# Optimization experiments

Hardware: AMD Instinct MI355X
Metric: run time of the kernel (lower is better)

The kernel has to match this reference:

```python
import jax, jax.numpy as jnp
import numpy as np

B, S, CIN, COUT, W, M, P = 32, 8192, 2, 1, 64, 16, 24


def setup_inputs() -> dict:
    key = jax.random.key(0)
    ks = jax.random.split(key, 12)

    def lin(k, o, i):
        return (jax.random.uniform(k, (o, i), jnp.float32) * 2 - 1) / np.float32(np.sqrt(i))

    scale = np.float32(1.0 / (W * W))  # SpectralConv1d init scale 1/(in*out)
    return {
        "x": jax.random.normal(ks[0], (B, S, CIN), jnp.float32),
        "fc0_w": lin(ks[1], W, CIN),
        "fc0_b": jnp.zeros((W,), jnp.float32),
        "conv_wr": jax.random.uniform(ks[2], (4, W, W, M), jnp.float32) * scale,
        "conv_wi": jax.random.uniform(ks[3], (4, W, W, M), jnp.float32) * scale,
        "pw_w": lin(ks[4], 4 * W, W).reshape(4, W, W),  # 1x1 conv weights (out,in)
        "pw_b": jnp.zeros((4, W), jnp.float32),
        "fc1_w": lin(ks[5], 128, W),
        "fc1_b": jnp.zeros((128,), jnp.float32),
        "fc2_w": lin(ks[6], COUT, 128),
        "ica_w": lin(ks[7], P, 128),
        "ica_b": jnp.zeros((P,), jnp.float32),
    }


def spectral_conv(h, wr, wi, n):
    # h: (B, W, S). Keep first M rfft modes, complex-multiply, inverse rfft.
    xf = jnp.fft.rfft(h, axis=-1)[..., :M]          # (B, W, M) complex
    w = wr + 1j * wi                                 # (W, W, M)
    of = jnp.einsum('bix,iox->box', xf, w)           # (B, W, M)
    of = jnp.pad(of, ((0, 0), (0, 0), (0, n // 2 + 1 - M)))
    return jnp.fft.irfft(of, n=n, axis=-1)


def reference(x, fc0_w, fc0_b, conv_wr, conv_wi, pw_w, pw_b, fc1_w, fc1_b, fc2_w, ica_w, ica_b):
    b, s, _ = x.shape
    h = x @ fc0_w.T + fc0_b                          # lift: (B, S, W)
    h = h.transpose(0, 2, 1)                         # (B, W, S)
    for l in range(4):
        x1 = spectral_conv(h, conv_wr[l], conv_wi[l], s)
        x2 = jnp.einsum('oi,bis->bos', pw_w[l], h) + pw_b[l][None, :, None]
        h = x1 + x2
        if l < 3:                                    # no relu after layer 3 (as in torch code)
            h = jax.nn.relu(h)
    h = h.transpose(0, 2, 1)                         # (B, S, W)
    h = h @ fc1_w.T + fc1_b                          # (B, S, 128)
    h_ = jax.nn.relu(h)
    # broadcast ICA decomposition: (B,S,1,128)*(1,1,COUT,128)
    components = h_[:, :, None, :] * fc2_w[None, None, :, :]
    tc = components @ ica_w.T + ica_b                # (B, S, COUT, P)
    out = tc.sum(-1)                                 # (B, S, COUT)
    return out, tc
```

## Files before the change

kernel.cpp:

```cpp
#include <hip/hip_runtime.h>
#include <math.h>

#define SB 8192
#define NB 32
#define WC 64
#define NM 16
#define NKC 32
#define NP 24
#define NSC 16
#define LP 132


__global__ __launch_bounds__(256) void k_table(float* __restrict__ T) {
    int s = blockIdx.x * 256 + threadIdx.x;
    float* row = T + (size_t)s * NKC;
    #pragma unroll
    for (int k = 0; k < NM; ++k) {
        int m = (k * s) & (SB - 1);
        double ang = (double)m * (6.283185307179586476925286766559 / (double)SB);
        row[2 * k]     = (float)cos(ang);
        row[2 * k + 1] = (float)sin(ang);
    }
}

__global__ __launch_bounds__(256) void k_prep(const float* __restrict__ ica_w,
                                              const float* __restrict__ fc2_w,
                                              float* __restrict__ icaT) {
    int tid = blockIdx.x * 256 + threadIdx.x;
    int c = tid / NP;
    int p = tid - c * NP;
    icaT[c * NP + p] = ica_w[p * 128 + c] * fc2_w[c];
}

__global__ __launch_bounds__(256) void k_prepw(const float* __restrict__ pw_w,
                                               float* __restrict__ pwT) {
    int tid = blockIdx.x * 256 + threadIdx.x;
    int l = tid >> 12, k = (tid >> 6) & 63, o = tid & 63;
    pwT[tid] = pw_w[(size_t)l * 4096 + o * 64 + k];
}

__global__ __launch_bounds__(256) void k_lift(const float* __restrict__ x,
                                              const float* __restrict__ fc0_w,
                                              const float* __restrict__ fc0_b,
                                              float* __restrict__ h) {
    int b = blockIdx.y;
    int s = blockIdx.x * 256 + threadIdx.x;
    float2 xv = ((const float2*)x)[(size_t)b * SB + s];
    #pragma unroll
    for (int w = 0; w < WC; ++w) {
        float v = fmaf(xv.x, fc0_w[2 * w], fmaf(xv.y, fc0_w[2 * w + 1], fc0_b[w]));
        h[((size_t)(b * WC + w)) * SB + s] = v;
    }
}

__global__ __launch_bounds__(256) void k_dft(const float* __restrict__ h,
                                             const float* __restrict__ T,
                                             float* __restrict__ xfp) {
    __shared__ float u[12800];
    int blk = blockIdx.x;
    int b  = blk >> 4;
    int sc = blk & (NSC - 1);
    int t  = threadIdx.x;
    int lane = t & 63;
    int wv = __builtin_amdgcn_readfirstlane(t >> 6);
    int g  = lane >> 3;
    int j8 = lane & 7;

    float acc[8][4];
    #pragma unroll
    for (int i = 0; i < 8; ++i)
        #pragma unroll
        for (int m = 0; m < 4; ++m) acc[i][m] = 0.f;

    int ch_s = t >> 2, part = t & 3;
    const float* hb = h + ((size_t)(b * WC + ch_s)) * SB;

    for (int st = 0; st < 4; ++st) {
        int s_base = sc * 512 + st * 128;

        const float* hrow = hb + s_base;
        #pragma unroll
        for (int r = 0; r < 8; ++r) {
            int so = (part + 4 * r) * 4;
            float4 v = *(const float4*)(hrow + so);
            u[(so + 0) * 68 + ch_s] = v.x;
            u[(so + 1) * 68 + ch_s] = v.y;
            u[(so + 2) * 68 + ch_s] = v.z;
            u[(so + 3) * 68 + ch_s] = v.w;
        }
        {
            const float4* tsrc = (const float4*)(T + (size_t)s_base * NKC);
            float4* tdst = (float4*)(u + 8704);
            #pragma unroll
            for (int r = 0; r < 4; ++r) tdst[t + r * 256] = tsrc[t + r * 256];
        }
        __syncthreads();

        #pragma unroll 4
        for (int ss = 0; ss < 32; ++ss) {
            int s = wv * 32 + ss;
            float4 tv = *(const float4*)&u[8704 + s * 32 + j8 * 4];
            float4 h0 = *(const float4*)&u[s * 68 + g * 8];
            float4 h1 = *(const float4*)&u[s * 68 + g * 8 + 4];
            float hh[8] = {h0.x, h0.y, h0.z, h0.w, h1.x, h1.y, h1.z, h1.w};
            #pragma unroll
            for (int i = 0; i < 8; ++i) {
                acc[i][0] = fmaf(hh[i], tv.x, acc[i][0]);
                acc[i][1] = fmaf(hh[i], tv.y, acc[i][1]);
                acc[i][2] = fmaf(hh[i], tv.z, acc[i][2]);
                acc[i][3] = fmaf(hh[i], tv.w, acc[i][3]);
            }
        }
        __syncthreads();
    }

    {
        float* slot = u + (wv * 64 + lane) * 33;
        #pragma unroll
        for (int i = 0; i < 8; ++i)
            #pragma unroll
            for (int m = 0; m < 4; ++m) slot[i * 4 + m] = acc[i][m];
    }
    __syncthreads();

    float* dst = xfp + ((size_t)(sc * NB + b)) * 2048;
    float res[8];
    #pragma unroll
    for (int e = 0; e < 8; ++e) {
        int idx = t * 8 + e;
        int ch = idx >> 5, mode = idx & 31;
        int g2 = ch >> 3, i2 = ch & 7;
        int q2 = mode >> 2, m2 = mode & 3;
        int lane2 = g2 * 8 + q2;
        int v2 = i2 * 4 + m2;
        res[e] = u[lane2 * 33 + v2] + u[(64 + lane2) * 33 + v2]
               + u[(128 + lane2) * 33 + v2] + u[(192 + lane2) * 33 + v2];
    }
    float4* d4 = (float4*)(dst + t * 8);
    d4[0] = make_float4(res[0], res[1], res[2], res[3]);
    d4[1] = make_float4(res[4], res[5], res[6], res[7]);
}

__global__ __launch_bounds__(256) void k_red(const float* __restrict__ xfp,
                                             float* __restrict__ xf) {
    int idx = blockIdx.x * 256 + threadIdx.x;
    int b = idx >> 11;
    int r = idx & 2047;
    float s = 0.f;
    #pragma unroll
    for (int sc = 0; sc < NSC; ++sc)
        s += xfp[((size_t)(sc * NB + b)) * 2048 + r];
    xf[idx] = s;
}

__global__ __launch_bounds__(256) void k_mix(const float* __restrict__ xf,
                                             const float* __restrict__ wr,
                                             const float* __restrict__ wi,
                                             float* __restrict__ ofT) {
    int tid = blockIdx.x * 256 + threadIdx.x;
    int k = tid & 15;
    int o = (tid >> 4) & 63;
    int b = tid >> 10;
    float orr = 0.f, oii = 0.f;
    const float2* xfb = (const float2*)(xf + (size_t)b * WC * NKC);
    #pragma unroll 4
    for (int i = 0; i < WC; ++i) {
        float2 cs = xfb[i * NM + k];
        float wrv = wr[(i * WC + o) * NM + k];
        float wiv = wi[(i * WC + o) * NM + k];
        orr = fmaf(cs.x, wrv, fmaf(cs.y, wiv, orr));
        oii = fmaf(cs.x, wiv, fmaf(-cs.y, wrv, oii));
    }
    float alpha = (k == 0 ? 1.f : 2.f) / (float)SB;
    ofT[((size_t)b * NKC + 2 * k) * 64 + o]     = alpha * orr;
    ofT[((size_t)b * NKC + 2 * k + 1) * 64 + o] = -alpha * oii;
}

__global__ __launch_bounds__(256) void k_update(float* __restrict__ h,
                                                const float* __restrict__ T,
                                                const float* __restrict__ ofT,
                                                const float* __restrict__ pwT,
                                                const float* __restrict__ pwb,
                                                int relu) {
    __shared__ float hS[96][LP];
    int t = threadIdx.x;
    int b = blockIdx.y;
    int s0 = blockIdx.x * 128;
    int lane_s = t & 63;
    int g = __builtin_amdgcn_readfirstlane((t >> 6) & 3);
    int ob = g * 16;

    {
        int ch = t >> 2, part = t & 3;
        const float* hrow = h + ((size_t)(b * WC + ch)) * SB + s0;
        #pragma unroll
        for (int r = 0; r < 8; ++r) {
            int so = (part + 4 * r) * 4;
            *(float4*)&hS[ch][so] = *(const float4*)(hrow + so);
        }
    }
    {
        int sl = t >> 1, jj0 = (t & 1) * 16;
        const float4* src = (const float4*)(T + (size_t)(s0 + sl) * NKC + jj0);
        float4 a = src[0], c4 = src[1], d = src[2], e = src[3];
        hS[64 + jj0 +  0][sl] = a.x;  hS[64 + jj0 +  1][sl] = a.y;
        hS[64 + jj0 +  2][sl] = a.z;  hS[64 + jj0 +  3][sl] = a.w;
        hS[64 + jj0 +  4][sl] = c4.x; hS[64 + jj0 +  5][sl] = c4.y;
        hS[64 + jj0 +  6][sl] = c4.z; hS[64 + jj0 +  7][sl] = c4.w;
        hS[64 + jj0 +  8][sl] = d.x;  hS[64 + jj0 +  9][sl] = d.y;
        hS[64 + jj0 + 10][sl] = d.z;  hS[64 + jj0 + 11][sl] = d.w;
        hS[64 + jj0 + 12][sl] = e.x;  hS[64 + jj0 + 13][sl] = e.y;
        hS[64 + jj0 + 14][sl] = e.z;  hS[64 + jj0 + 15][sl] = e.w;
    }
    __syncthreads();

    float acc0[16], acc1[16];
    #pragma unroll
    for (int o = 0; o < 16; ++o) { acc0[o] = pwb[ob + o]; acc1[o] = pwb[ob + o]; }

    const float* wbase0 = pwT + ob;
    const float* wbase1 = ofT + ((size_t)b * NKC) * 64 + ob;

    for (int kc = 0; kc < 8; ++kc) {
        #pragma unroll
        for (int u = 0; u < 8; ++u) {
            int k = kc * 8 + u;
            float h0 = hS[k][lane_s];
            float h1 = hS[k][64 + lane_s];
            const float* w = wbase0 + k * 64;
            #pragma unroll
            for (int o = 0; o < 16; ++o) {
                acc0[o] = fmaf(w[o], h0, acc0[o]);
                acc1[o] = fmaf(w[o], h1, acc1[o]);
            }
        }
    }
    for (int kc = 0; kc < 4; ++kc) {
        #pragma unroll
        for (int u = 0; u < 8; ++u) {
            int j = kc * 8 + u;
            float h0 = hS[64 + j][lane_s];
            float h1 = hS[64 + j][64 + lane_s];
            const float* w = wbase1 + j * 64;
            #pragma unroll
            for (int o = 0; o < 16; ++o) {
                acc0[o] = fmaf(w[o], h0, acc0[o]);
                acc1[o] = fmaf(w[o], h1, acc1[o]);
            }
        }
    }

    float* hw0 = h + (size_t)b * WC * SB + s0 + lane_s;
    float* hw1 = hw0 + 64;
    #pragma unroll
    for (int o = 0; o < 16; ++o) {
        float v0 = acc0[o], v1 = acc1[o];
        if (relu) { v0 = fmaxf(v0, 0.f); v1 = fmaxf(v1, 0.f); }
        hw0[(size_t)(ob + o) * SB] = v0;
        hw1[(size_t)(ob + o) * SB] = v1;
    }
}

__global__ __launch_bounds__(256) void k_final(const float* __restrict__ h,
                                               const float* __restrict__ fc1_w,
                                               const float* __restrict__ fc1_b,
                                               const float* __restrict__ icaT,
                                               const float* __restrict__ ica_b,
                                               float* __restrict__ out,
                                               float* __restrict__ tc) {
    __shared__ float u_lds[6400];
    float (*hS)[68] = (float(*)[68])u_lds;
    int t = threadIdx.x;
    int b = blockIdx.y;
    int s0 = blockIdx.x * 64;
    int lane_s = t & 63;
    int wv = __builtin_amdgcn_readfirstlane(t >> 6);
    int c0 = wv * 32;

    {
        int sl = t & 63, chg = t >> 6;
        const float* hb = h + (size_t)b * WC * SB + s0 + sl;
        #pragma unroll
        for (int cc = 0; cc < 16; ++cc) {
            int ch = chg * 16 + cc;
            hS[sl][ch] = hb[(size_t)ch * SB];
        }
    }
    __syncthreads();

    float acc[NP];
    #pragma unroll
    for (int p = 0; p < NP; ++p) acc[p] = 0.f;

    for (int cq = 0; cq < 8; ++cq) {
        int c = c0 + 4 * cq;
        float tv0 = fc1_b[c], tv1 = fc1_b[c + 1], tv2 = fc1_b[c + 2], tv3 = fc1_b[c + 3];
        const float* w0 = fc1_w + (size_t)c * WC;
        const float* w1 = w0 + WC;
        const float* w2 = w1 + WC;
        const float* w3 = w2 + WC;
        for (int ioct = 0; ioct < 8; ++ioct) {
            float4 xa = *(const float4*)&hS[lane_s][ioct * 8];
            float4 xb = *(const float4*)&hS[lane_s][ioct * 8 + 4];
            float xs[8] = {xa.x, xa.y, xa.z, xa.w, xb.x, xb.y, xb.z, xb.w};
            #pragma unroll
            for (int u = 0; u < 8; ++u) {
                int i = ioct * 8 + u;
                tv0 = fmaf(w0[i], xs[u], tv0);
                tv1 = fmaf(w1[i], xs[u], tv1);
                tv2 = fmaf(w2[i], xs[u], tv2);
                tv3 = fmaf(w3[i], xs[u], tv3);
            }
        }
        tv0 = fmaxf(tv0, 0.f); tv1 = fmaxf(tv1, 0.f);
        tv2 = fmaxf(tv2, 0.f); tv3 = fmaxf(tv3, 0.f);
        const float* e0 = icaT + (size_t)c * NP;
        const float* e1 = e0 + NP;
        const float* e2 = e1 + NP;
        const float* e3 = e2 + NP;
        #pragma unroll
        for (int p = 0; p < NP; ++p)
            acc[p] = fmaf(tv0, e0[p], fmaf(tv1, e1[p],
                     fmaf(tv2, e2[p], fmaf(tv3, e3[p], acc[p]))));
    }

    __syncthreads();
    {
        float* slot = u_lds + ((t >> 6) * 64 + lane_s) * 25;
        #pragma unroll
        for (int p = 0; p < NP; ++p) slot[p] = acc[p];
    }
    __syncthreads();

    float* tcb = tc + ((size_t)b * SB + s0) * NP;
    #pragma unroll
    for (int r = 0; r < 6; ++r) {
        int e = t + r * 256;
        int s = e / NP, p = e - s * NP;
        float v = u_lds[s * 25 + p] + u_lds[(64 + s) * 25 + p]
                + u_lds[(128 + s) * 25 + p] + u_lds[(192 + s) * 25 + p]
                + ica_b[p];
        tcb[e] = v;
        u_lds[s * 25 + p] = v;
    }
    __syncthreads();
    if (t < 64) {
        float osum = 0.f;
        #pragma unroll
        for (int p = 0; p < NP; ++p) osum += u_lds[t * 25 + p];
        out[(size_t)b * SB + s0 + t] = osum;
    }
}

extern "C" void kernel_launch(void* const* d_in, const int* in_sizes, int n_in,
                              void* d_out, int out_size, void* d_ws, size_t ws_size,
                              hipStream_t stream) {
    const float* x     = (const float*)d_in[0];
    const float* fc0_w = (const float*)d_in[1];
    const float* fc0_b = (const float*)d_in[2];
    const float* cwr   = (const float*)d_in[3];
    const float* cwi   = (const float*)d_in[4];
    const float* pw_w  = (const float*)d_in[5];
    const float* pw_b  = (const float*)d_in[6];
    const float* fc1_w = (const float*)d_in[7];
    const float* fc1_b = (const float*)d_in[8];
    const float* fc2_w = (const float*)d_in[9];
    const float* ica_w = (const float*)d_in[10];
    const float* ica_b = (const float*)d_in[11];

    float* out = (float*)d_out;
    float* tc  = out + (size_t)NB * SB;

    float* ws   = (float*)d_ws;
    float* h    = ws;
    float* T    = ws + 16777216;
    float* xf   = ws + 17039360;
    float* ofT  = ws + 17104896;
    float* icaT = ws + 17170432;
    float* pwT  = ws + 17173504;
    float* xfp  = tc;

    k_table<<<32, 256, 0, stream>>>(T);
    k_prep<<<12, 256, 0, stream>>>(ica_w, fc2_w, icaT);
    k_prepw<<<64, 256, 0, stream>>>(pw_w, pwT);
    k_lift<<<dim3(32, 32), 256, 0, stream>>>(x, fc0_w, fc0_b, h);

    for (int l = 0; l < 4; ++l) {
        k_dft<<<NB * NSC, 256, 0, stream>>>(h, T, xfp);
        k_red<<<256, 256, 0, stream>>>(xfp, xf);
        k_mix<<<128, 256, 0, stream>>>(xf, cwr + (size_t)l * WC * WC * NM,
                                       cwi + (size_t)l * WC * WC * NM, ofT);
        k_update<<<dim3(64, 32), 256, 0, stream>>>(h, T, ofT,
                                                   pwT + (size_t)l * 4096,
                                                   pw_b + (size_t)l * WC,
                                                   (l < 3) ? 1 : 0);
    }

    k_final<<<dim3(128, 32), 256, 0, stream>>>(h, fc1_w, fc1_b, icaT, ica_b, out, tc);
}
```

Measured before the change: 434.8 us.

## Fuse forward DFT partial sums into k_update epilogue for next layer

For layers 0-2, k_update now stages its freshly computed h tile in LDS after writing it out. It then computes the 16-mode DFT partial sums for its 128-sample chunk and writes them to xfp. This removes the separate k_dft launch for layers 1-3 and its re-read of the full h tensor from global memory. k_red now takes a variable chunk count (64 instead of 16) to reduce the finer-grained partials. The cost is more LDS work and syncs per block and a larger partial-sum buffer to read.

```diff
diff --git a/kernel.cpp b/kernel.cpp
--- a/kernel.cpp
+++ b/kernel.cpp
@@ -142,13 +142,13 @@
 }
 
 __global__ __launch_bounds__(256) void k_red(const float* __restrict__ xfp,
-                                             float* __restrict__ xf) {
+                                             float* __restrict__ xf, int nsc) {
     int idx = blockIdx.x * 256 + threadIdx.x;
     int b = idx >> 11;
     int r = idx & 2047;
     float s = 0.f;
-    #pragma unroll
-    for (int sc = 0; sc < NSC; ++sc)
+    #pragma unroll 8
+    for (int sc = 0; sc < nsc; ++sc)
         s += xfp[((size_t)(sc * NB + b)) * 2048 + r];
     xf[idx] = s;
 }
@@ -181,14 +181,16 @@
                                                 const float* __restrict__ ofT,
                                                 const float* __restrict__ pwT,
                                                 const float* __restrict__ pwb,
-                                                int relu) {
-    __shared__ float hS[96][LP];
+                                                int relu, float* __restrict__ xfp,
+                                                int dodft) {
+    __shared__ float u[96 * LP];
+    float (*hS)[LP] = (float(*)[LP])u;
     int t = threadIdx.x;
     int b = blockIdx.y;
     int s0 = blockIdx.x * 128;
     int lane_s = t & 63;
-    int g = __builtin_amdgcn_readfirstlane((t >> 6) & 3);
-    int ob = g * 16;
+    int g4 = __builtin_amdgcn_readfirstlane((t >> 6) & 3);
+    int ob = g4 * 16;
 
     {
         int ch = t >> 2, part = t & 3;
@@ -223,8 +225,8 @@
 
     for (int kc = 0; kc < 8; ++kc) {
         #pragma unroll
-        for (int u = 0; u < 8; ++u) {
-            int k = kc * 8 + u;
+        for (int uu = 0; uu < 8; ++uu) {
+            int k = kc * 8 + uu;
             float h0 = hS[k][lane_s];
             float h1 = hS[k][64 + lane_s];
             const float* w = wbase0 + k * 64;
@@ -237,8 +239,8 @@
     }
     for (int kc = 0; kc < 4; ++kc) {
         #pragma unroll
-        for (int u = 0; u < 8; ++u) {
-            int j = kc * 8 + u;
+        for (int uu = 0; uu < 8; ++uu) {
+            int j = kc * 8 + uu;
             float h0 = hS[64 + j][lane_s];
             float h1 = hS[64 + j][64 + lane_s];
             const float* w = wbase1 + j * 64;
@@ -250,15 +252,88 @@
         }
     }
 
+    if (relu) {
+        #pragma unroll
+        for (int o = 0; o < 16; ++o) {
+            acc0[o] = fmaxf(acc0[o], 0.f);
+            acc1[o] = fmaxf(acc1[o], 0.f);
+        }
+    }
+
     float* hw0 = h + (size_t)b * WC * SB + s0 + lane_s;
     float* hw1 = hw0 + 64;
     #pragma unroll
     for (int o = 0; o < 16; ++o) {
-        float v0 = acc0[o], v1 = acc1[o];
-        if (relu) { v0 = fmaxf(v0, 0.f); v1 = fmaxf(v1, 0.f); }
-        hw0[(size_t)(ob + o) * SB] = v0;
-        hw1[(size_t)(ob + o) * SB] = v1;
-    }
+        hw0[(size_t)(ob + o) * SB] = acc0[o];
+        hw1[(size_t)(ob + o) * SB] = acc1[o];
+    }
+
+    if (!dodft) return;
+
+    __syncthreads();
+    #pragma unroll
+    for (int o = 0; o < 16; ++o) {
+        u[lane_s * 65 + ob + o]        = acc0[o];
+        u[(64 + lane_s) * 65 + ob + o] = acc1[o];
+    }
+    __syncthreads();
+
+    int lane = t & 63;
+    int wv = __builtin_amdgcn_readfirstlane(t >> 6);
+    int g  = lane >> 3;
+    int j8 = lane & 7;
+
+    float dacc[8][4];
+    #pragma unroll
+    for (int i = 0; i < 8; ++i)
+        #pragma unroll
+        for (int m = 0; m < 4; ++m) dacc[i][m] = 0.f;
+
+    #pragma unroll 4
+    for (int ss = 0; ss < 32; ++ss) {
+        int s = wv * 32 + ss;
+        float tv0 = u[64 * LP + (j8 * 4 + 0) * LP + s];
+        float tv1 = u[64 * LP + (j8 * 4 + 1) * LP + s];
+        float tv2 = u[64 * LP + (j8 * 4 + 2) * LP + s];
+        float tv3 = u[64 * LP + (j8 * 4 + 3) * LP + s];
+        float4 h0 = *(const float4*)&u[s * 65 + g * 8];
+        float4 h1 = *(const float4*)&u[s * 65 + g * 8 + 4];
+        float hh[8] = {h0.x, h0.y, h0.z, h0.w, h1.x, h1.y, h1.z, h1.w};
+        #pragma unroll
+        for (int i = 0; i < 8; ++i) {
+            dacc[i][0] = fmaf(hh[i], tv0, dacc[i][0]);
+            dacc[i][1] = fmaf(hh[i], tv1, dacc[i][1]);
+            dacc[i][2] = fmaf(hh[i], tv2, dacc[i][2]);
+            dacc[i][3] = fmaf(hh[i], tv3, dacc[i][3]);
+        }
+    }
+
+    __syncthreads();
+    {
+        float* slot = u + (wv * 64 + lane) * 33;
+        #pragma unroll
+        for (int i = 0; i < 8; ++i)
+            #pragma unroll
+            for (int m = 0; m < 4; ++m) slot[i * 4 + m] = dacc[i][m];
+    }
+    __syncthreads();
+
+    float* dst = xfp + ((size_t)(blockIdx.x * NB + b)) * 2048;
+    float res[8];
+    #pragma unroll
+    for (int e = 0; e < 8; ++e) {
+        int idx = t * 8 + e;
+        int ch = idx >> 5, mode = idx & 31;
+        int g2 = ch >> 3, i2 = ch & 7;
+        int q2 = mode >> 2, m2 = mode & 3;
+        int lane2 = g2 * 8 + q2;
+        int v2 = i2 * 4 + m2;
+        res[e] = u[lane2 * 33 + v2] + u[(64 + lane2) * 33 + v2]
+               + u[(128 + lane2) * 33 + v2] + u[(192 + lane2) * 33 + v2];
+    }
+    float4* d4 = (float4*)(dst + t * 8);
+    d4[0] = make_float4(res[0], res[1], res[2], res[3]);
+    d4[1] = make_float4(res[4], res[5], res[6], res[7]);
 }
 
 __global__ __launch_bounds__(256) void k_final(const float* __restrict__ h,
@@ -304,12 +379,12 @@
             float4 xb = *(const float4*)&hS[lane_s][ioct * 8 + 4];
             float xs[8] = {xa.x, xa.y, xa.z, xa.w, xb.x, xb.y, xb.z, xb.w};
             #pragma unroll
-            for (int u = 0; u < 8; ++u) {
-                int i = ioct * 8 + u;
-                tv0 = fmaf(w0[i], xs[u], tv0);
-                tv1 = fmaf(w1[i], xs[u], tv1);
-                tv2 = fmaf(w2[i], xs[u], tv2);
-                tv3 = fmaf(w3[i], xs[u], tv3);
+            for (int uu = 0; uu < 8; ++uu) {
+                int i = ioct * 8 + uu;
+                tv0 = fmaf(w0[i], xs[uu], tv0);
+                tv1 = fmaf(w1[i], xs[uu], tv1);
+                tv2 = fmaf(w2[i], xs[uu], tv2);
+                tv3 = fmaf(w3[i], xs[uu], tv3);
             }
         }
         tv0 = fmaxf(tv0, 0.f); tv1 = fmaxf(tv1, 0.f);
@@ -386,14 +461,19 @@
     k_lift<<<dim3(32, 32), 256, 0, stream>>>(x, fc0_w, fc0_b, h);
 
     for (int l = 0; l < 4; ++l) {
-        k_dft<<<NB * NSC, 256, 0, stream>>>(h, T, xfp);
-        k_red<<<256, 256, 0, stream>>>(xfp, xf);
+        if (l == 0) {
+            k_dft<<<NB * NSC, 256, 0, stream>>>(h, T, xfp);
+            k_red<<<256, 256, 0, stream>>>(xfp, xf, NSC);
+        } else {
+            k_red<<<256, 256, 0, stream>>>(xfp, xf, 64);
+        }
         k_mix<<<128, 256, 0, stream>>>(xf, cwr + (size_t)l * WC * WC * NM,
                                        cwi + (size_t)l * WC * WC * NM, ofT);
         k_update<<<dim3(64, 32), 256, 0, stream>>>(h, T, ofT,
                                                    pwT + (size_t)l * 4096,
                                                    pw_b + (size_t)l * WC,
-                                                   (l < 3) ? 1 : 0);
+                                                   (l < 3) ? 1 : 0,
+                                                   xfp, (l < 3) ? 1 : 0);
     }
 
     k_final<<<dim3(128, 32), 256, 0, stream>>>(h, fc1_w, fc1_b, icaT, ica_b, out, tc);
```

After: 425.8 us. -2.1%, faster.
